# Kernel tuning notes

Hardware: AMD Instinct MI355X
Metric: run time of the kernel (lower is better)

## Reference

```python
import jax, jax.numpy as jnp
import numpy as np

# dims
B, V, IMG = 16, 2, 224
G, PATCH, SG = 7, 14, 16
D, NH, L = 768, 12, 12
DH = D // NH            # 64
P = DH // 4             # rope frequencies per axis (2D axial RoPE)
N = G * G               # 49 glimpse tokens
S = SG * SG             # 256 scene tokens
GSIZE = G * PATCH       # 98 px glimpse


def _ln(x, w, b):
    m = x.mean(-1, keepdims=True)
    v = ((x - m) ** 2).mean(-1, keepdims=True)
    return (x - m) * jax.lax.rsqrt(v + 1e-6) * w + b


def _rope(pos, periods):
    # pos [B,N,2] -> cos,sin [B,N,2P]  (x freqs then y freqs)
    ang = (pos[..., :, None] / periods).reshape(pos.shape[0], pos.shape[1], -1)
    return jnp.cos(ang), jnp.sin(ang)


def _apply_rope(x, cos, sin):
    # x [B,H,N,DH]; cos/sin [B,N,DH//2]
    c = cos[:, None, :, :]
    s = sin[:, None, :, :]
    xr = x.reshape(x.shape[0], x.shape[1], x.shape[2], DH // 2, 2)
    x1, x2 = xr[..., 0], xr[..., 1]
    return jnp.stack([x1 * c - x2 * s, x1 * s + x2 * c], -1).reshape(x.shape)


def _heads(x):
    return x.reshape(x.shape[0], x.shape[1], NH, DH).transpose(0, 2, 1, 3)


def _merge(x):
    return x.transpose(0, 2, 1, 3).reshape(x.shape[0], x.shape[2], D)


def _attn(q, k, v):
    a = jax.nn.softmax(jnp.einsum('bhqd,bhkd->bhqk', q, k) / jnp.sqrt(jnp.float32(DH)), axis=-1)
    return jnp.einsum('bhqk,bhkd->bhqd', a, v)


def _cross(xq, xkv, qw, qb, kvw, kvb, ow, ob, rq, rkv):
    q = _heads(xq @ qw.T + qb)
    kv = xkv @ kvw.T + kvb
    k, v = _heads(kv[..., :D]), _heads(kv[..., D:])
    q = _apply_rope(q, *rq)
    k = _apply_rope(k, *rkv)
    return _merge(_attn(q, k, v)) @ ow.T + ob


def _bilinear(img, py, px):
    # img [C,H,W], py/px [GSIZE] pixel coords -> [C,GSIZE,GSIZE]
    Hh, Ww = img.shape[1], img.shape[2]
    y0 = jnp.clip(jnp.floor(py), 0, Hh - 2).astype(jnp.int32)
    x0 = jnp.clip(jnp.floor(px), 0, Ww - 2).astype(jnp.int32)
    wy = jnp.clip(py - y0, 0.0, 1.0)[None, :, None]
    wx = jnp.clip(px - x0, 0.0, 1.0)[None, None, :]
    g0, g1 = img[:, y0, :], img[:, y0 + 1, :]
    v00, v01 = g0[:, :, x0], g0[:, :, x0 + 1]
    v10, v11 = g1[:, :, x0], g1[:, :, x0 + 1]
    return (v00 * (1 - wy) + v10 * wy) * (1 - wx) + (v01 * (1 - wy) + v11 * wy) * wx


def _extract(images, c, s):
    # crop a [-1,1]-normalized glimpse of half-width `scale` at `center`
    lin = jnp.linspace(-1.0, 1.0, GSIZE)
    gy = c[:, 1:2] + s[:, None] * lin
    gx = c[:, 0:1] + s[:, None] * lin
    py = (gy + 1.0) * 0.5 * (images.shape[2] - 1)
    px = (gx + 1.0) * 0.5 * (images.shape[3] - 1)
    return jax.vmap(_bilinear)(images, py, px)


def _forward(images, centers, scales, patch_w, patch_b, scene_tokens,
             ln1_w, ln1_b, ln2_w, ln2_b, qkv_w, qkv_b, attn_out_w, attn_out_b,
             mlp_w1, mlp_b1, mlp_w2, mlp_b2,
             read_q_w, read_q_b, read_kv_w, read_kv_b, read_out_w, read_out_b, read_gate,
             write_q_w, write_q_b, write_kv_w, write_kv_b, write_out_w, write_out_b, write_gate):
    periods = 100.0 ** (jnp.arange(P, dtype=jnp.float32) / P)
    lin_s = jnp.linspace(-1.0, 1.0, SG)
    ys, xs = jnp.meshgrid(lin_s, lin_s, indexing='ij')
    scene_pos = jnp.broadcast_to(jnp.stack([xs.ravel(), ys.ravel()], -1), (B, S, 2))
    scene_rope = _rope(scene_pos, periods)
    lin_g = jnp.linspace(-1.0, 1.0, G)
    yg, xg = jnp.meshgrid(lin_g, lin_g, indexing='ij')
    goffs = jnp.stack([xg.ravel(), yg.ravel()], -1)  # [N,2]

    scene = jnp.broadcast_to(scene_tokens, (B, S, D))
    for vp in range(V):
        glimpse = _extract(images, centers[vp], scales[vp])  # [B,3,98,98]
        t = jax.lax.conv_general_dilated(glimpse, patch_w, (PATCH, PATCH), 'VALID',
                                         dimension_numbers=('NCHW', 'OIHW', 'NCHW'))
        local = t.reshape(B, D, N).transpose(0, 2, 1) + patch_b  # [B,49,D]
        lpos = centers[vp][:, None, :] + scales[vp][:, None, None] * goffs
        lrope = _rope(lpos, periods)
        for i in range(L):
            local = local + read_gate[i] * _cross(local, scene,
                read_q_w[i], read_q_b[i], read_kv_w[i], read_kv_b[i],
                read_out_w[i], read_out_b[i], lrope, scene_rope)
            # ViT block with RoPE self-attention
            h = _ln(local, ln1_w[i], ln1_b[i])
            qkv = h @ qkv_w[i].T + qkv_b[i]
            q, k, v = _heads(qkv[..., :D]), _heads(qkv[..., D:2 * D]), _heads(qkv[..., 2 * D:])
            q = _apply_rope(q, *lrope)
            k = _apply_rope(k, *lrope)
            local = local + _merge(_attn(q, k, v)) @ attn_out_w[i].T + attn_out_b[i]
            h = _ln(local, ln2_w[i], ln2_b[i])
            local = local + jax.nn.gelu(h @ mlp_w1[i].T + mlp_b1[i]) @ mlp_w2[i].T + mlp_b2[i]
            scene = scene + write_gate[i] * _cross(scene, local,
                write_q_w[i], write_q_b[i], write_kv_w[i], write_kv_b[i],
                write_out_w[i], write_out_b[i], scene_rope, lrope)
    return scene  # [B,S,D]


def setup_inputs() -> dict:
    key = jax.random.key(0)
    ks = iter(jax.random.split(key, 40))
    std = 0.02
    d = {}
    d['images'] = jax.random.normal(next(ks), (B, 3, IMG, IMG), jnp.float32)
    d['centers'] = jax.random.uniform(next(ks), (V, B, 2), jnp.float32, -0.5, 0.5)
    d['scales'] = jax.random.uniform(next(ks), (V, B), jnp.float32, 0.2, 0.4)
    d['patch_w'] = jax.random.normal(next(ks), (D, 3, PATCH, PATCH), jnp.float32) * std
    d['patch_b'] = jnp.zeros((D,), jnp.float32)
    d['scene_tokens'] = jax.random.normal(next(ks), (1, S, D), jnp.float32) / jnp.sqrt(jnp.float32(D))
    d['ln1_w'] = jnp.ones((L, D), jnp.float32); d['ln1_b'] = jnp.zeros((L, D), jnp.float32)
    d['ln2_w'] = jnp.ones((L, D), jnp.float32); d['ln2_b'] = jnp.zeros((L, D), jnp.float32)
    d['qkv_w'] = jax.random.normal(next(ks), (L, 3 * D, D), jnp.float32) * std
    d['qkv_b'] = jnp.zeros((L, 3 * D), jnp.float32)
    d['attn_out_w'] = jax.random.normal(next(ks), (L, D, D), jnp.float32) * std
    d['attn_out_b'] = jnp.zeros((L, D), jnp.float32)
    d['mlp_w1'] = jax.random.normal(next(ks), (L, 4 * D, D), jnp.float32) * std
    d['mlp_b1'] = jnp.zeros((L, 4 * D), jnp.float32)
    d['mlp_w2'] = jax.random.normal(next(ks), (L, D, 4 * D), jnp.float32) * std
    d['mlp_b2'] = jnp.zeros((L, D), jnp.float32)
    for pre in ('read', 'write'):
        d[pre + '_q_w'] = jax.random.normal(next(ks), (L, D, D), jnp.float32) * std
        d[pre + '_q_b'] = jnp.zeros((L, D), jnp.float32)
        d[pre + '_kv_w'] = jax.random.normal(next(ks), (L, 2 * D, D), jnp.float32) * std
        d[pre + '_kv_b'] = jnp.zeros((L, 2 * D), jnp.float32)
        d[pre + '_out_w'] = jax.random.normal(next(ks), (L, D, D), jnp.float32) * std
        d[pre + '_out_b'] = jnp.zeros((L, D), jnp.float32)
        d[pre + '_gate'] = jax.random.normal(next(ks), (L, D), jnp.float32) * 0.1
    return d


def reference(images, centers, scales, patch_w, patch_b, scene_tokens,
              ln1_w, ln1_b, ln2_w, ln2_b, qkv_w, qkv_b, attn_out_w, attn_out_b,
              mlp_w1, mlp_b1, mlp_w2, mlp_b2,
              read_q_w, read_q_b, read_kv_w, read_kv_b, read_out_w, read_out_b, read_gate,
              write_q_w, write_q_b, write_kv_w, write_kv_b, write_out_w, write_out_b, write_gate):
    return _forward(images, centers, scales, patch_w, patch_b, scene_tokens,
                    ln1_w, ln1_b, ln2_w, ln2_b, qkv_w, qkv_b, attn_out_w, attn_out_b,
                    mlp_w1, mlp_b1, mlp_w2, mlp_b2,
                    read_q_w, read_q_b, read_kv_w, read_kv_b, read_out_w, read_out_b, read_gate,
                    write_q_w, write_q_b, write_kv_w, write_kv_b, write_out_w, write_out_b, write_gate)
```

## Files before the change

kernel.cpp:

```cpp
#include <hip/hip_runtime.h>

#define B_ 16
#define V_ 2
#define D_ 768
#define NH_ 12
#define L_ 12
#define DH_ 64
#define N_ 49
#define S_ 256

__device__ __forceinline__ unsigned short f2bf(float f) {
  unsigned int u = __builtin_bit_cast(unsigned int, f);
  u += 0x7fffu + ((u >> 16) & 1u);
  return (unsigned short)(u >> 16);
}
__device__ __forceinline__ float bf2f(unsigned short h) {
  unsigned int u = ((unsigned int)h) << 16;
  return __builtin_bit_cast(float, u);
}
__device__ __forceinline__ float bflo(unsigned int w) {
  return __builtin_bit_cast(float, w << 16);
}
__device__ __forceinline__ float bfhi(unsigned int w) {
  return __builtin_bit_cast(float, w & 0xffff0000u);
}
__device__ __forceinline__ unsigned int packbf2(float a, float b) {
  return (unsigned int)f2bf(a) | ((unsigned int)f2bf(b) << 16);
}

using bf16x8 = __attribute__((ext_vector_type(8))) __bf16;
using u16x8  = __attribute__((ext_vector_type(8))) unsigned short;
using f32x4  = __attribute__((ext_vector_type(4))) float;

__device__ __forceinline__ void g2l16(const unsigned short* g, unsigned short* l) {
  __builtin_amdgcn_global_load_lds(
      (const __attribute__((address_space(1))) unsigned int*)g,
      (__attribute__((address_space(3))) unsigned int*)l, 16, 0, 0);
}

template <int BM, int BN, int BK, bool SWZ>
__global__ __launch_bounds__(256) void gemm_v7(
    const unsigned short* __restrict__ A, int lda,
    const unsigned short* __restrict__ W, int ldw,
    const float* __restrict__ bias,
    float* __restrict__ Cf, unsigned short* __restrict__ Cb, int ldc,
    const float* __restrict__ res, const float* __restrict__ gate,
    float* __restrict__ stats,
    int M, int N, int K, int epi)
{
  __shared__ unsigned short As[2][BM * BK];
  __shared__ unsigned short Bs[2][BN * BK];
  constexpr int FM = BM / 32, FN = BN / 32;
  constexpr int CPR = BK / 8;
  constexpr int LPS = (BM + BN) * BK / 2048;
  int m0, n0;
  if (SWZ) {
    const int gx = gridDim.x;
    const int nwg = gx * gridDim.y;
    const int orig = blockIdx.y * gx + blockIdx.x;
    const int xcd = orig & 7, rem = orig >> 3;
    const int qq = nwg >> 3, rr = nwg & 7;
    const int wgid = (xcd < rr ? xcd * (qq + 1) : rr * (qq + 1) + (xcd - rr) * qq) + rem;
    m0 = (wgid % gx) * BM; n0 = (wgid / gx) * BN;
  } else {
    m0 = blockIdx.x * BM; n0 = blockIdx.y * BN;
  }
  const int tid = threadIdx.x, lane = tid & 63, wid = tid >> 6;
  const int wr = wid >> 1, wc = wid & 1;
  const int fr = lane & 15, kq8 = lane >> 4;

  f32x4 acc[FM][FN];
#pragma unroll
  for (int mi = 0; mi < FM; ++mi)
#pragma unroll
    for (int ni = 0; ni < FN; ++ni) acc[mi][ni] = f32x4{0.f, 0.f, 0.f, 0.f};

  auto stage = [&](int buf, int k0) {
    const unsigned short* Ab = A + (size_t)m0 * lda + k0;
    const unsigned short* Bb = W + (size_t)n0 * ldw + k0;
#pragma unroll
    for (int ra = 0; ra < BM * BK / 2048; ++ra) {
      int c = ra * 256 + tid;
      int row = c / CPR, slot = c % CPR;
      int gslot = slot ^ (row & 7);
      g2l16(Ab + (size_t)row * lda + gslot * 8, &As[buf][c * 8]);
    }
#pragma unroll
    for (int rb = 0; rb < BN * BK / 2048; ++rb) {
      int c = rb * 256 + tid;
      int row = c / CPR, slot = c % CPR;
      int gslot = slot ^ (row & 7);
      g2l16(Bb + (size_t)row * ldw + gslot * 8, &Bs[buf][c * 8]);
    }
  };

  const int nt = K / BK;
  stage(0, 0);
  int cur = 0;
  for (int t = 0; t < nt; ++t) {
    if (t + 1 < nt) {
      stage(cur ^ 1, (t + 1) * BK);
      asm volatile("s_waitcnt vmcnt(%0)" :: "i"(LPS) : "memory");
    } else {
      asm volatile("s_waitcnt vmcnt(0)" ::: "memory");
    }
    __builtin_amdgcn_s_barrier();
#pragma unroll
    for (int ks = 0; ks < BK / 32; ++ks) {
      bf16x8 av[FM], bv[FN];
#pragma unroll
      for (int mi = 0; mi < FM; ++mi) {
        int row = wr * (BM / 2) + mi * 16 + fr;
        int idx = row * BK + (((ks * 4 + kq8) ^ (row & 7)) << 3);
        av[mi] = __builtin_bit_cast(bf16x8, *(const u16x8*)&As[cur][idx]);
      }
#pragma unroll
      for (int ni = 0; ni < FN; ++ni) {
        int row = wc * (BN / 2) + ni * 16 + fr;
        int idx = row * BK + (((ks * 4 + kq8) ^ (row & 7)) << 3);
        bv[ni] = __builtin_bit_cast(bf16x8, *(const u16x8*)&Bs[cur][idx]);
      }
#pragma unroll
      for (int mi = 0; mi < FM; ++mi)
#pragma unroll
        for (int ni = 0; ni < FN; ++ni)
          acc[mi][ni] = __builtin_amdgcn_mfma_f32_16x16x32_bf16(av[mi], bv[ni], acc[mi][ni], 0, 0, 0);
    }
    __builtin_amdgcn_s_barrier();
    cur ^= 1;
  }

  const int er = (lane >> 4) * 4, ec = lane & 15;
#pragma unroll
  for (int mi = 0; mi < FM; ++mi) {
#pragma unroll
    for (int i = 0; i < 4; ++i) {
      int gr = m0 + wr * (BM / 2) + mi * 16 + er + i;
      float mu = 0.f, rs = 0.f;
      if (epi >= 3) {
        float su = stats[gr * 2], sq = stats[gr * 2 + 1];
        mu = su * (1.0f / 768.0f);
        rs = rsqrtf(fmaxf(sq * (1.0f / 768.0f) - mu * mu, 0.f) + 1e-6f);
      }
      float s = 0.f, q = 0.f;
#pragma unroll
      for (int ni = 0; ni < FN; ++ni) {
        int gc = n0 + wc * (BN / 2) + ni * 16 + ec;
        float bi = bias ? bias[gc] : 0.0f;
        float gg = gate ? gate[gc] : 1.0f;
        float v = acc[mi][ni][i];
        if (epi == 0) {
          v += bi;
        } else if (epi == 1) {
          v += bi;
          v = v / (1.0f + __expf(-1.59576912f * (v + 0.044715f * v * v * v)));
        } else if (epi == 2) {
          v += bi;
          if (gr < M) v = res[(size_t)gr * ldc + gc] + gg * v;
        } else {
          v = (v - mu * gg) * rs + bi;
          if (epi == 4)
            v = v / (1.0f + __expf(-1.59576912f * (v + 0.044715f * v * v * v)));
        }
        if (gr < M) {
          if (Cf) Cf[(size_t)gr * ldc + gc] = v;
          if (Cb) Cb[(size_t)gr * ldc + gc] = f2bf(v);
        }
        s += v; q += v * v;
      }
      if (epi == 2 && stats) {
#pragma unroll
        for (int off = 1; off <= 8; off <<= 1) {
          s += __shfl_xor(s, off);
          q += __shfl_xor(q, off);
        }
        if ((lane & 15) == 0 && gr < M) {
          atomicAdd(&stats[gr * 2], s);
          atomicAdd(&stats[gr * 2 + 1], q);
        }
      }
    }
  }
}

template <int LKPAD>
__global__ __launch_bounds__(256) void attn_mfma(
    const unsigned short* __restrict__ Q, int ldq, int qoff, int Lq,
    const unsigned short* __restrict__ KV, int ldkv, int koff, int voff, int Lk,
    const float* __restrict__ cq, const float* __restrict__ sq, int rbq,
    const float* __restrict__ ck, const float* __restrict__ sk, int rbk,
    unsigned short* __restrict__ Out)
{
  constexpr int NT = LKPAD / 16;
  constexpr int NKS = LKPAD / 32;
  __shared__ unsigned short Kb[LKPAD * 64];
  __shared__ unsigned short Vt[64 * LKPAD];
  __shared__ unsigned short Qs[4][16 * 64];
  __shared__ unsigned short Pl[4][16 * LKPAD];
  const int b = blockIdx.x / NH_, h = blockIdx.x - b * NH_;
  const int tid = threadIdx.x, lane = tid & 63, wid = tid >> 6;

  for (int idx = tid; idx < LKPAD * 32; idx += 256) {
    int t = idx >> 5, m = idx & 31;
    int d = 2 * m;
    int ksl = (t << 6) + (((m >> 2) ^ (t & 7)) << 3) + ((m & 3) << 1);
    int vs0 = d * LKPAD + (((t >> 3) ^ (d & 7)) << 3) + (t & 7);
    int vs1 = (d + 1) * LKPAD + (((t >> 3) ^ ((d + 1) & 7)) << 3) + (t & 7);
    if (t < Lk) {
      size_t rowb = ((size_t)b * Lk + t) * ldkv;
      unsigned int kw = *(const unsigned int*)(KV + rowb + koff + h * DH_ + d);
      unsigned int vw = *(const unsigned int*)(KV + rowb + voff + h * DH_ + d);
      float k1 = bflo(kw), k2 = bfhi(kw);
      size_t ri = (size_t)b * rbk + (size_t)t * 32 + m;
      float c = ck[ri], s = sk[ri];
      *(unsigned int*)&Kb[ksl] = packbf2((k1 * c - k2 * s) * 0.125f, (k1 * s + k2 * c) * 0.125f);
      Vt[vs0] = (unsigned short)(vw & 0xffff);
      Vt[vs1] = (unsigned short)(vw >> 16);
    } else {
      *(unsigned int*)&Kb[ksl] = 0;
      Vt[vs0] = 0; Vt[vs1] = 0;
    }
  }
  const int qbase = blockIdx.y * 64 + wid * 16;
  for (int idx = lane; idx < 16 * 32; idx += 64) {
    int r = idx >> 5, m = idx & 31;
    int gq = qbase + r;
    unsigned int qr = 0;
    if (gq < Lq) {
      unsigned int qw = *(const unsigned int*)(Q + ((size_t)b * Lq + gq) * ldq + qoff + h * DH_ + 2 * m);
      float q1 = bflo(qw), q2 = bfhi(qw);
      size_t ri = (size_t)b * rbq + (size_t)gq * 32 + m;
      float c = cq[ri], s = sq[ri];
      qr = packbf2(q1 * c - q2 * s, q1 * s + q2 * c);
    }
    *(unsigned int*)&Qs[wid][(r << 6) + (((m >> 2) ^ (r & 7)) << 3) + ((m & 3) << 1)] = qr;
  }
  __syncthreads();

  const int fr = lane & 15, g = lane >> 4;
  bf16x8 qa[2];
#pragma unroll
  for (int ks = 0; ks < 2; ++ks)
    qa[ks] = __builtin_bit_cast(bf16x8,
        *(const u16x8*)&Qs[wid][(fr << 6) + ((((ks << 2) + g) ^ (fr & 7)) << 3)]);

  f32x4 sv[NT];
  __builtin_amdgcn_s_setprio(1);
#pragma unroll
  for (int t = 0; t < NT; ++t) {
    int key = (t << 4) + fr;
    f32x4 a = {0.f, 0.f, 0.f, 0.f};
#pragma unroll
    for (int ks = 0; ks < 2; ++ks) {
      bf16x8 kb = __builtin_bit_cast(bf16x8,
          *(const u16x8*)&Kb[(key << 6) + ((((ks << 2) + g) ^ (key & 7)) << 3)]);
      a = __builtin_amdgcn_mfma_f32_16x16x32_bf16(qa[ks], kb, a, 0, 0, 0);
    }
    sv[t] = a;
  }
  __builtin_amdgcn_s_setprio(0);
#pragma unroll
  for (int t = 0; t < NT; ++t) {
    int key = (t << 4) + fr;
    if (key >= Lk) sv[t] = f32x4{-1e30f, -1e30f, -1e30f, -1e30f};
  }
  f32x4 mx = sv[0];
#pragma unroll
  for (int t = 1; t < NT; ++t)
#pragma unroll
    for (int i = 0; i < 4; ++i) mx[i] = fmaxf(mx[i], sv[t][i]);
#pragma unroll
  for (int off = 1; off <= 8; off <<= 1)
#pragma unroll
    for (int i = 0; i < 4; ++i) mx[i] = fmaxf(mx[i], __shfl_xor(mx[i], off));
  f32x4 sm = {0.f, 0.f, 0.f, 0.f};
#pragma unroll
  for (int t = 0; t < NT; ++t)
#pragma unroll
    for (int i = 0; i < 4; ++i) {
      float e = __expf(sv[t][i] - mx[i]);
      sv[t][i] = e;
      sm[i] += e;
    }
#pragma unroll
  for (int off = 1; off <= 8; off <<= 1)
#pragma unroll
    for (int i = 0; i < 4; ++i) sm[i] += __shfl_xor(sm[i], off);
  f32x4 inv;
#pragma unroll
  for (int i = 0; i < 4; ++i) inv[i] = 1.0f / sm[i];
#pragma unroll
  for (int t = 0; t < NT; ++t) {
    int key = (t << 4) + fr;
    int chunk = key >> 3;
#pragma unroll
    for (int i = 0; i < 4; ++i) {
      int row = (g << 2) + i;
      Pl[wid][row * LKPAD + ((chunk ^ (row & 7)) << 3) + (key & 7)] = f2bf(sv[t][i]);
    }
  }
  f32x4 oacc[4];
#pragma unroll
  for (int n = 0; n < 4; ++n) oacc[n] = f32x4{0.f, 0.f, 0.f, 0.f};
  __builtin_amdgcn_s_setprio(1);
#pragma unroll
  for (int ks = 0; ks < NKS; ++ks) {
    int chunk = (ks << 2) + g;
    bf16x8 pa = __builtin_bit_cast(bf16x8,
        *(const u16x8*)&Pl[wid][fr * LKPAD + ((chunk ^ (fr & 7)) << 3)]);
#pragma unroll
    for (int n = 0; n < 4; ++n) {
      int drow = (n << 4) + fr;
      bf16x8 vb = __builtin_bit_cast(bf16x8,
          *(const u16x8*)&Vt[drow * LKPAD + ((chunk ^ (drow & 7)) << 3)]);
      oacc[n] = __builtin_amdgcn_mfma_f32_16x16x32_bf16(pa, vb, oacc[n], 0, 0, 0);
    }
  }
  __builtin_amdgcn_s_setprio(0);
#pragma unroll
  for (int n = 0; n < 4; ++n)
#pragma unroll
    for (int i = 0; i < 4; ++i) {
      int gq = qbase + (g << 2) + i;
      if (gq < Lq)
        Out[((size_t)b * Lq + gq) * D_ + h * DH_ + (n << 4) + fr] = f2bf(oacc[n][i] * inv[i]);
    }
}

struct CvtA {
  const float* s[11];
  unsigned short* d[11];
  const float* g[11];
  unsigned int lsrc[11];
  unsigned int lstride[11];
  int blkEnd[11];
};
__global__ __launch_bounds__(256) void cvt_multi_k(CvtA c) {
  int bid = blockIdx.x;
  int seg = 0;
#pragma unroll
  for (int i = 0; i < 10; ++i) seg += (bid >= c.blkEnd[i]) ? 1 : 0;
  unsigned int e = (unsigned int)(bid - (seg ? c.blkEnd[seg - 1] : 0)) * 2048u
                   + (unsigned int)threadIdx.x * 8u;
  unsigned int l = e / c.lsrc[seg], r = e - l * c.lsrc[seg];
  const float* s = c.s[seg] + e;
  unsigned short* d = c.d[seg] + (size_t)l * c.lstride[seg] + r;
  f32x4 a = *(const f32x4*)s, b2 = *(const f32x4*)(s + 4);
  const float* gp = c.g[seg];
  if (gp) {
    unsigned int k = e % 768u;
    const float* gpp = gp + (size_t)l * 768u + k;
    f32x4 ga = *(const f32x4*)gpp, gb = *(const f32x4*)(gpp + 4);
    a.x *= ga.x; a.y *= ga.y; a.z *= ga.z; a.w *= ga.w;
    b2.x *= gb.x; b2.y *= gb.y; b2.z *= gb.z; b2.w *= gb.w;
  }
  u16x8 o;
  o[0] = f2bf(a.x); o[1] = f2bf(a.y); o[2] = f2bf(a.z); o[3] = f2bf(a.w);
  o[4] = f2bf(b2.x); o[5] = f2bf(b2.y); o[6] = f2bf(b2.z); o[7] = f2bf(b2.w);
  *(u16x8*)d = o;
}

__global__ __launch_bounds__(256) void foldprep_k(
    const float* __restrict__ qkvw, const float* __restrict__ qkvb,
    const float* __restrict__ g1, const float* __restrict__ b1,
    const float* __restrict__ m1w, const float* __restrict__ m1b,
    const float* __restrict__ g2, const float* __restrict__ b2,
    float* __restrict__ cq, float* __restrict__ bq,
    float* __restrict__ cm, float* __restrict__ bm)
{
  int row = blockIdx.x * 4 + (threadIdx.x >> 6);
  int lane = threadIdx.x & 63;
  const int QT = L_ * 2304;
  const float *wrow, *gv, *bv;
  float bb; float *co, *bo; int oi;
  if (row < QT) {
    int l = row / 2304, n = row - l * 2304;
    wrow = qkvw + ((size_t)l * 2304 + n) * 768;
    gv = g1 + l * 768; bv = b1 + l * 768;
    bb = qkvb[row]; co = cq; bo = bq; oi = row;
  } else {
    int r2 = row - QT;
    int l = r2 / 3072, n = r2 - l * 3072;
    wrow = m1w + ((size_t)l * 3072 + n) * 768;
    gv = g2 + l * 768; bv = b2 + l * 768;
    bb = m1b[r2]; co = cm; bo = bm; oi = r2;
  }
  float cs = 0.f, bs = 0.f;
#pragma unroll
  for (int j = 0; j < 12; ++j) {
    float w = wrow[lane + 64 * j];
    cs += w * gv[lane + 64 * j];
    bs += w * bv[lane + 64 * j];
  }
  for (int o = 32; o; o >>= 1) { cs += __shfl_xor(cs, o); bs += __shfl_xor(bs, o); }
  if (lane == 0) { co[oi] = cs; bo[oi] = bb + bs; }
}

__global__ void cvt_patch_k(const float* __restrict__ s, unsigned short* __restrict__ d) {
  int i = blockIdx.x * 256 + threadIdx.x;
  if (i >= 768 * 768) return;
  int r = i / 768, col = i - r * 768;
  d[i] = f2bf(col < 588 ? s[r * 588 + col] : 0.0f);
}

__global__ void fbias_k(const float* __restrict__ wqb, const float* __restrict__ rkvb,
                        float* __restrict__ fb) {
  int i = blockIdx.x * 256 + threadIdx.x;
  if (i >= L_ * 2304) return;
  int l = i / 2304, c = i - l * 2304;
  fb[i] = (c < 768) ? wqb[l * 768 + c] : rkvb[l * 1536 + (c - 768)];
}

__global__ void fbias2_k(const float* __restrict__ wkvb, const float* __restrict__ rqb,
                         float* __restrict__ fb2) {
  int i = blockIdx.x * 256 + threadIdx.x;
  if (i >= L_ * 2304) return;
  int l = i / 2304, c = i - l * 2304;
  fb2[i] = (c < 1536) ? wkvb[l * 1536 + c] : rqb[((l + 1) % L_) * 768 + (c - 1536)];
}

__global__ void init_scene_k(const float* __restrict__ tok, float* __restrict__ sf,
                             unsigned short* __restrict__ sb, int total) {
  int i = blockIdx.x * 256 + threadIdx.x;
  if (i < total) {
    float v = tok[i % (S_ * D_)];
    sf[i] = v; sb[i] = f2bf(v);
  }
}

__global__ void rope_scene_k(float* __restrict__ c, float* __restrict__ s) {
  int idx = blockIdx.x * 256 + threadIdx.x;
  if (idx >= S_ * 32) return;
  int t = idx >> 5, m = idx & 31;
  int i = t >> 4, j = t & 15;
  float xx = -1.0f + 2.0f * j / 15.0f;
  float yy = -1.0f + 2.0f * i / 15.0f;
  float coord = (m < 16) ? xx : yy;
  float per = powf(100.0f, (float)(m & 15) / 16.0f);
  float ang = coord / per;
  c[idx] = cosf(ang); s[idx] = sinf(ang);
}

__global__ void rope_local_k(float* __restrict__ c, float* __restrict__ s,
                             const float* __restrict__ ctr, const float* __restrict__ scl) {
  int idx = blockIdx.x * 256 + threadIdx.x;
  if (idx >= B_ * N_ * 32) return;
  int b = idx / (N_ * 32);
  int r = idx - b * (N_ * 32);
  int pch = r >> 5, m = r & 31;
  int py = pch / 7, px = pch - py * 7;
  float cx = ctr[b * 2], cy = ctr[b * 2 + 1], sc = scl[b];
  float gx = cx + sc * ((px - 3.0f) / 3.0f);
  float gy = cy + sc * ((py - 3.0f) / 3.0f);
  float coord = (m < 16) ? gx : gy;
  float per = powf(100.0f, (float)(m & 15) / 16.0f);
  float ang = coord / per;
  c[idx] = cosf(ang); s[idx] = sinf(ang);
}

__global__ void im2col_k(unsigned short* __restrict__ xb, const float* __restrict__ img,
                         const float* __restrict__ ctr, const float* __restrict__ scl) {
  int idx = blockIdx.x * 256 + threadIdx.x;
  if (idx >= 784 * 768) return;
  int row = idx / 768, col = idx - row * 768;
  float val = 0.0f;
  if (col < 588) {
    int b = row / 49, pch = row - b * 49;
    int c = col / 196, rr = col - c * 196;
    int i = rr / 14, j = rr - i * 14;
    int py = pch / 7, px = pch - py * 7;
    int gyi = py * 14 + i, gxi = px * 14 + j;
    float cx = ctr[b * 2], cy = ctr[b * 2 + 1], sc = scl[b];
    float gy = cy + sc * (-1.0f + 2.0f * gyi / 97.0f);
    float gx = cx + sc * (-1.0f + 2.0f * gxi / 97.0f);
    float pyi = (gy + 1.0f) * 0.5f * 223.0f;
    float pxi = (gx + 1.0f) * 0.5f * 223.0f;
    float y0f = fminf(fmaxf(floorf(pyi), 0.0f), 222.0f);
    float x0f = fminf(fmaxf(floorf(pxi), 0.0f), 222.0f);
    int y0 = (int)y0f, x0 = (int)x0f;
    float wy = fminf(fmaxf(pyi - y0f, 0.0f), 1.0f);
    float wx = fminf(fmaxf(pxi - x0f, 0.0f), 1.0f);
    const float* base = img + (size_t)(b * 3 + c) * 224 * 224;
    float v00 = base[y0 * 224 + x0],       v01 = base[y0 * 224 + x0 + 1];
    float v10 = base[(y0 + 1) * 224 + x0], v11 = base[(y0 + 1) * 224 + x0 + 1];
    val = (v00 * (1.0f - wy) + v10 * wy) * (1.0f - wx) + (v01 * (1.0f - wy) + v11 * wy) * wx;
  }
  xb[idx] = f2bf(val);
}

extern "C" void kernel_launch(void* const* d_in, const int* in_sizes, int n_in,
                              void* d_out, int out_size, void* d_ws, size_t ws_size,
                              hipStream_t stream) {
  const float* images    = (const float*)d_in[0];
  const float* centers   = (const float*)d_in[1];
  const float* scales    = (const float*)d_in[2];
  const float* patch_w   = (const float*)d_in[3];
  const float* patch_b   = (const float*)d_in[4];
  const float* scene_tok = (const float*)d_in[5];
  const float* ln1_w = (const float*)d_in[6];
  const float* ln1_b = (const float*)d_in[7];
  const float* ln2_w = (const float*)d_in[8];
  const float* ln2_b = (const float*)d_in[9];
  const float* qkv_w = (const float*)d_in[10];
  const float* qkv_b = (const float*)d_in[11];
  const float* ao_w  = (const float*)d_in[12];
  const float* ao_b  = (const float*)d_in[13];
  const float* m1_w  = (const float*)d_in[14];
  const float* m1_b  = (const float*)d_in[15];
  const float* m2_w  = (const float*)d_in[16];
  const float* m2_b  = (const float*)d_in[17];
  const float* rq_w  = (const float*)d_in[18];
  const float* rq_b  = (const float*)d_in[19];
  const float* rkv_w = (const float*)d_in[20];
  const float* rkv_b = (const float*)d_in[21];
  const float* ro_w  = (const float*)d_in[22];
  const float* ro_b  = (const float*)d_in[23];
  const float* rgate = (const float*)d_in[24];
  const float* wq_w  = (const float*)d_in[25];
  const float* wq_b  = (const float*)d_in[26];
  const float* wkv_w = (const float*)d_in[27];
  const float* wkv_b = (const float*)d_in[28];
  const float* wo_w  = (const float*)d_in[29];
  const float* wo_b  = (const float*)d_in[30];
  const float* wgate = (const float*)d_in[31];

  float* scene_f = (float*)d_out;

  char* p = (char*)d_ws;
  auto alloc = [&](size_t bytes) { char* r = p; p += (bytes + 255) & ~(size_t)255; return (void*)r; };
  unsigned short* scene_bf = (unsigned short*)alloc((size_t)4096 * 768 * 2);
  float*          local_f  = (float*)alloc((size_t)784 * 768 * 4);
  unsigned short* local_bf = (unsigned short*)alloc((size_t)896 * 768 * 2);
  unsigned short* q_r_bf   = (unsigned short*)alloc((size_t)896 * 768 * 2);
  unsigned short* qrkv_bf  = (unsigned short*)alloc((size_t)4096 * 2304 * 2);
  unsigned short* kv_bf    = (unsigned short*)alloc((size_t)896 * 2304 * 2);
  unsigned short* kvq_bf   = (unsigned short*)alloc((size_t)896 * 2304 * 2);
  unsigned short* act_bf   = (unsigned short*)alloc((size_t)4096 * 768 * 2);
  unsigned short* x_bf     = (unsigned short*)alloc((size_t)896 * 768 * 2);
  float* sc_cos = (float*)alloc((size_t)S_ * 32 * 4);
  float* sc_sin = (float*)alloc((size_t)S_ * 32 * 4);
  float* l_cos  = (float*)alloc((size_t)B_ * N_ * 32 * 4);
  float* l_sin  = (float*)alloc((size_t)B_ * N_ * 32 * 4);
  unsigned short* patch_wbf = (unsigned short*)alloc((size_t)768 * 768 * 2);
  float*          fb        = (float*)alloc((size_t)L_ * 2304 * 4);
  float*          fb2       = (float*)alloc((size_t)L_ * 2304 * 4);
  float*          cq_v      = (float*)alloc((size_t)L_ * 2304 * 4);
  float*          bq_v      = (float*)alloc((size_t)L_ * 2304 * 4);
  float*          cm_v      = (float*)alloc((size_t)L_ * 3072 * 4);
  float*          bm_v      = (float*)alloc((size_t)L_ * 3072 * 4);
  const size_t ST_SLICE = 896 * 2;
  float*          statsAll  = (float*)alloc((size_t)V_ * L_ * 2 * ST_SLICE * 4);

  static const size_t REGSZ[9] = {589824, 1769472, 589824, 1769472, 589824,
                                  2359296, 2359296, 1769472, 589824};
  struct SegDef { const float* src; int reg; unsigned off; unsigned lsrc; int nl; const float* gma; };
  const SegDef SEGS[11] = {
    {rq_w,            0, 0,       589824,  L_,    nullptr},
    {wq_w,            1, 0,       589824,  L_,    nullptr},
    {rkv_w,           1, 589824,  1179648, L_,    nullptr},
    {ro_w,            2, 0,       589824,  L_,    nullptr},
    {qkv_w,           3, 0,       1769472, L_,    ln1_w},
    {ao_w,            4, 0,       589824,  L_,    nullptr},
    {m1_w,            5, 0,       2359296, L_,    ln2_w},
    {m2_w,            6, 0,       2359296, L_,    nullptr},
    {wkv_w,           7, 0,       1179648, L_,    nullptr},
    {rq_w + 589824,   7, 1179648, 589824,  L_ - 1, nullptr},
    {wo_w,            8, 0,       589824,  L_,    nullptr},
  };
  size_t regBase[9];
  size_t perLayer = 0;
  {
    size_t cur = 0;
    for (int i = 0; i < 9; ++i) { regBase[i] = cur; cur += REGSZ[i] * L_; perLayer += REGSZ[i]; }
  }
  const size_t allElems = perLayer * L_;
  size_t usedBytes = (size_t)(p - (char*)d_ws);
  bool preconv = ws_size >= usedBytes + allElems * 2 + 4096;
  unsigned short* wbf = (unsigned short*)alloc((preconv ? allElems : perLayer) * 2);

  auto GQ = [&](const unsigned short* A, int lda, const unsigned short* Wp,
                const float* bias, float* Cf, unsigned short* Cb, int ldc,
                const float* res, const float* gt, int N, int epi) {
    gemm_v7<128, 128, 64, true><<<dim3(32, N / 128), 256, 0, stream>>>(
        A, lda, Wp, 768, bias, Cf, Cb, ldc, res, gt, nullptr, 4096, N, 768, epi);
  };
  auto GW = [&](const unsigned short* A, int lda, const unsigned short* Wp,
                const float* bias, float* Cf, unsigned short* Cb, int ldc,
                const float* res, const float* gt, int N, int epi) {
    gemm_v7<128, 64, 64, true><<<dim3(32, N / 64), 256, 0, stream>>>(
        A, lda, Wp, 768, bias, Cf, Cb, ldc, res, gt, nullptr, 4096, N, 768, epi);
  };
  auto GS = [&](const unsigned short* A, int lda, const unsigned short* Wp, int ldw,
                const float* bias, float* Cf, unsigned short* Cb, int ldc,
                const float* res, const float* gt, float* st, int N, int K, int epi) {
    gemm_v7<64, 64, 128, false><<<dim3(13, N / 64), 256, 0, stream>>>(
        A, lda, Wp, ldw, bias, Cf, Cb, ldc, res, gt, st, 784, N, K, epi);
  };

  {
    hipMemsetAsync(statsAll, 0, (size_t)V_ * L_ * 2 * ST_SLICE * 4, stream);
    int total = B_ * S_ * D_;
    init_scene_k<<<(total + 255) / 256, 256, 0, stream>>>(scene_tok, scene_f, scene_bf, total);
    rope_scene_k<<<(S_ * 32 + 255) / 256, 256, 0, stream>>>(sc_cos, sc_sin);
    cvt_patch_k<<<(768 * 768 + 255) / 256, 256, 0, stream>>>(patch_w, patch_wbf);
    fbias_k<<<(L_ * 2304 + 255) / 256, 256, 0, stream>>>(wq_b, rkv_b, fb);
    fbias2_k<<<(L_ * 2304 + 255) / 256, 256, 0, stream>>>(wkv_b, rq_b, fb2);
    foldprep_k<<<(L_ * (2304 + 3072)) / 4, 256, 0, stream>>>(
        qkv_w, qkv_b, ln1_w, ln1_b, m1_w, m1_b, ln2_w, ln2_b, cq_v, bq_v, cm_v, bm_v);
    if (preconv) {
      CvtA cv;
      int blk = 0;
      for (int i = 0; i < 11; ++i) {
        cv.s[i] = SEGS[i].src;
        cv.d[i] = wbf + regBase[SEGS[i].reg] + SEGS[i].off;
        cv.g[i] = SEGS[i].gma;
        cv.lsrc[i] = SEGS[i].lsrc;
        cv.lstride[i] = (unsigned)REGSZ[SEGS[i].reg];
        blk += (int)((size_t)SEGS[i].lsrc * SEGS[i].nl / 2048);
        cv.blkEnd[i] = blk;
      }
      cvt_multi_k<<<blk, 256, 0, stream>>>(cv);
    }
  }

  for (int vp = 0; vp < V_; ++vp) {
    const float* ctr = centers + (size_t)vp * B_ * 2;
    const float* scl = scales + (size_t)vp * B_;
    rope_local_k<<<(B_ * N_ * 32 + 255) / 256, 256, 0, stream>>>(l_cos, l_sin, ctr, scl);
    im2col_k<<<(784 * 768 + 255) / 256, 256, 0, stream>>>(x_bf, images, ctr, scl);
    GS(x_bf, 768, patch_wbf, 768, patch_b, local_f, local_bf, 768,
       nullptr, nullptr, nullptr, 768, 768, 0);

    for (int l = 0; l < L_; ++l) {
      const unsigned short* wR[9];
      if (preconv) {
        for (int rg = 0; rg < 9; ++rg)
          wR[rg] = wbf + regBase[rg] + (size_t)l * REGSZ[rg];
      } else {
        CvtA cv;
        int blk = 0;
        size_t cur = 0;
        size_t rb[9];
        for (int rg = 0; rg < 9; ++rg) { rb[rg] = cur; cur += REGSZ[rg]; wR[rg] = wbf + rb[rg]; }
        for (int i = 0; i < 11; ++i) {
          size_t srcl = (i == 9) ? (size_t)((l + 1) % L_) : (size_t)l;
          cv.s[i] = (i == 9 ? rq_w : SEGS[i].src) + srcl * SEGS[i].lsrc;
          cv.d[i] = wbf + rb[SEGS[i].reg] + SEGS[i].off;
          cv.g[i] = SEGS[i].gma ? SEGS[i].gma + srcl * 768 : nullptr;
          cv.lsrc[i] = SEGS[i].lsrc;
          cv.lstride[i] = (unsigned)REGSZ[SEGS[i].reg];
          blk += (int)(SEGS[i].lsrc / 2048);
          cv.blkEnd[i] = blk;
        }
        cvt_multi_k<<<blk, 256, 0, stream>>>(cv);
      }
      float* stats1 = statsAll + ((size_t)(vp * L_ + l) * 2 + 0) * ST_SLICE;
      float* stats2 = statsAll + ((size_t)(vp * L_ + l) * 2 + 1) * ST_SLICE;

      GQ(scene_bf, 768, wR[1], fb + (size_t)l * 2304,
         nullptr, qrkv_bf, 2304, nullptr, nullptr, 2304, 0);
      if (l == 0)
        GS(local_bf, 768, wR[0], 768, rq_b + l * 768,
           nullptr, q_r_bf, 768, nullptr, nullptr, nullptr, 768, 768, 0);
      if (l == 0)
        attn_mfma<256><<<dim3(B_ * NH_, 1), 256, 0, stream>>>(q_r_bf, 768, 0, 49,
            qrkv_bf, 2304, 768, 1536, 256, l_cos, l_sin, N_ * 32, sc_cos, sc_sin, 0, act_bf);
      else
        attn_mfma<256><<<dim3(B_ * NH_, 1), 256, 0, stream>>>(kvq_bf, 2304, 1536, 49,
            qrkv_bf, 2304, 768, 1536, 256, l_cos, l_sin, N_ * 32, sc_cos, sc_sin, 0, act_bf);
      GS(act_bf, 768, wR[2], 768, ro_b + l * 768,
         local_f, local_bf, 768, local_f, rgate + l * 768, stats1, 768, 768, 2);
      GS(local_bf, 768, wR[3], 768, bq_v + (size_t)l * 2304,
         nullptr, kv_bf, 2304, nullptr, cq_v + (size_t)l * 2304, stats1, 2304, 768, 3);
      attn_mfma<64><<<dim3(B_ * NH_, 1), 256, 0, stream>>>(kv_bf, 2304, 0, 49,
          kv_bf, 2304, 768, 1536, 49, l_cos, l_sin, N_ * 32, l_cos, l_sin, N_ * 32, act_bf);
      GS(act_bf, 768, wR[4], 768, ao_b + l * 768,
         local_f, local_bf, 768, local_f, nullptr, stats2, 768, 768, 2);
      GS(local_bf, 768, wR[5], 768, bm_v + (size_t)l * 3072,
         nullptr, act_bf, 3072, nullptr, cm_v + (size_t)l * 3072, stats2, 3072, 768, 4);
      GS(act_bf, 3072, wR[6], 3072, m2_b + l * 768,
         local_f, local_bf, 768, local_f, nullptr, nullptr, 768, 3072, 2);
      GS(local_bf, 768, wR[7], 768, fb2 + (size_t)l * 2304,
         nullptr, kvq_bf, 2304, nullptr, nullptr, nullptr, 2304, 768, 0);
      attn_mfma<64><<<dim3(B_ * NH_, 4), 256, 0, stream>>>(qrkv_bf, 2304, 0, 256,
          kvq_bf, 2304, 0, 768, 49, sc_cos, sc_sin, 0, l_cos, l_sin, N_ * 32, act_bf);
      GW(act_bf, 768, wR[8], wo_b + l * 768,
         scene_f, scene_bf, 768, scene_f, wgate + l * 768, 768, 2);
    }
  }
}
```

Measured before the change: 6.919 ms.

## Specialize GEMM epilogues at compile time and replace stats atomics with partial slots

Turns the GEMM epilogue selector into a template parameter so each launch compiles only its own branch. Per-row LayerNorm sum and sum-of-squares partials now go into per-column-block slots with plain stores, and the consumer sums them, replacing atomicAdd and the stats memset. The RoPE table for the local tokens is now computed inside the im2col kernel, removing one launch per view. XCD swizzle is enabled for the small GEMMs too, at the cost of more kernel instantiations and wider stats reads in the normalizing epilogues.

```diff
diff --git a/kernel.cpp b/kernel.cpp
--- a/kernel.cpp
+++ b/kernel.cpp
@@ -38,7 +38,7 @@
       (__attribute__((address_space(3))) unsigned int*)l, 16, 0, 0);
 }
 
-template <int BM, int BN, int BK, bool SWZ>
+template <int BM, int BN, int BK, int EPI>
 __global__ __launch_bounds__(256) void gemm_v7(
     const unsigned short* __restrict__ A, int lda,
     const unsigned short* __restrict__ W, int ldw,
@@ -46,7 +46,7 @@
     float* __restrict__ Cf, unsigned short* __restrict__ Cb, int ldc,
     const float* __restrict__ res, const float* __restrict__ gate,
     float* __restrict__ stats,
-    int M, int N, int K, int epi)
+    int M, int N, int K)
 {
   __shared__ unsigned short As[2][BM * BK];
   __shared__ unsigned short Bs[2][BN * BK];
@@ -54,7 +54,7 @@
   constexpr int CPR = BK / 8;
   constexpr int LPS = (BM + BN) * BK / 2048;
   int m0, n0;
-  if (SWZ) {
+  {
     const int gx = gridDim.x;
     const int nwg = gx * gridDim.y;
     const int orig = blockIdx.y * gx + blockIdx.x;
@@ -62,8 +62,6 @@
     const int qq = nwg >> 3, rr = nwg & 7;
     const int wgid = (xcd < rr ? xcd * (qq + 1) : rr * (qq + 1) + (xcd - rr) * qq) + rem;
     m0 = (wgid % gx) * BM; n0 = (wgid / gx) * BN;
-  } else {
-    m0 = blockIdx.x * BM; n0 = blockIdx.y * BN;
   }
   const int tid = threadIdx.x, lane = tid & 63, wid = tid >> 6;
   const int wr = wid >> 1, wc = wid & 1;
@@ -82,15 +80,13 @@
     for (int ra = 0; ra < BM * BK / 2048; ++ra) {
       int c = ra * 256 + tid;
       int row = c / CPR, slot = c % CPR;
-      int gslot = slot ^ (row & 7);
-      g2l16(Ab + (size_t)row * lda + gslot * 8, &As[buf][c * 8]);
+      g2l16(Ab + (size_t)row * lda + (slot ^ (row & 7)) * 8, &As[buf][c * 8]);
     }
 #pragma unroll
     for (int rb = 0; rb < BN * BK / 2048; ++rb) {
       int c = rb * 256 + tid;
       int row = c / CPR, slot = c % CPR;
-      int gslot = slot ^ (row & 7);
-      g2l16(Bb + (size_t)row * ldw + gslot * 8, &Bs[buf][c * 8]);
+      g2l16(Bb + (size_t)row * ldw + (slot ^ (row & 7)) * 8, &Bs[buf][c * 8]);
     }
   };
 
@@ -131,55 +127,84 @@
   }
 
   const int er = (lane >> 4) * 4, ec = lane & 15;
-#pragma unroll
-  for (int mi = 0; mi < FM; ++mi) {
-#pragma unroll
-    for (int i = 0; i < 4; ++i) {
-      int gr = m0 + wr * (BM / 2) + mi * 16 + er + i;
-      float mu = 0.f, rs = 0.f;
-      if (epi >= 3) {
-        float su = stats[gr * 2], sq = stats[gr * 2 + 1];
-        mu = su * (1.0f / 768.0f);
-        rs = rsqrtf(fmaxf(sq * (1.0f / 768.0f) - mu * mu, 0.f) + 1e-6f);
+  float mu_[FM][4], rs_[FM][4];
+  if constexpr (EPI >= 4) {
+#pragma unroll
+    for (int mi = 0; mi < FM; ++mi)
+#pragma unroll
+      for (int i = 0; i < 4; ++i) {
+        int gr = m0 + wr * (BM / 2) + mi * 16 + er + i;
+        float su = 0.f, sq = 0.f;
+        if (gr < M) {
+          const f32x4* sp = (const f32x4*)&stats[(size_t)gr * 48];
+#pragma unroll
+          for (int j = 0; j < 12; ++j) {
+            f32x4 v4 = sp[j];
+            su += v4.x + v4.z;
+            sq += v4.y + v4.w;
+          }
+        }
+        float mu = su * (1.0f / 768.0f);
+        mu_[mi][i] = mu;
+        rs_[mi][i] = rsqrtf(fmaxf(sq * (1.0f / 768.0f) - mu * mu, 0.f) + 1e-6f);
       }
-      float s = 0.f, q = 0.f;
-#pragma unroll
-      for (int ni = 0; ni < FN; ++ni) {
-        int gc = n0 + wc * (BN / 2) + ni * 16 + ec;
-        float bi = bias ? bias[gc] : 0.0f;
-        float gg = gate ? gate[gc] : 1.0f;
+  }
+  float ssum[FM][4], sqsum[FM][4];
+  if constexpr (EPI == 3) {
+#pragma unroll
+    for (int mi = 0; mi < FM; ++mi)
+#pragma unroll
+      for (int i = 0; i < 4; ++i) { ssum[mi][i] = 0.f; sqsum[mi][i] = 0.f; }
+  }
+#pragma unroll
+  for (int mi = 0; mi < FM; ++mi)
+#pragma unroll
+    for (int ni = 0; ni < FN; ++ni) {
+      int gc = n0 + wc * (BN / 2) + ni * 16 + ec;
+      float bi = bias ? bias[gc] : 0.0f;
+      float gg = gate ? gate[gc] : 1.0f;
+#pragma unroll
+      for (int i = 0; i < 4; ++i) {
+        int gr = m0 + wr * (BM / 2) + mi * 16 + er + i;
         float v = acc[mi][ni][i];
-        if (epi == 0) {
+        if constexpr (EPI == 0) {
           v += bi;
-        } else if (epi == 1) {
+        } else if constexpr (EPI == 1) {
           v += bi;
           v = v / (1.0f + __expf(-1.59576912f * (v + 0.044715f * v * v * v)));
-        } else if (epi == 2) {
+        } else if constexpr (EPI == 2 || EPI == 3) {
           v += bi;
           if (gr < M) v = res[(size_t)gr * ldc + gc] + gg * v;
         } else {
-          v = (v - mu * gg) * rs + bi;
-          if (epi == 4)
+          v = (v - mu_[mi][i] * gg) * rs_[mi][i] + bi;
+          if constexpr (EPI == 5)
             v = v / (1.0f + __expf(-1.59576912f * (v + 0.044715f * v * v * v)));
         }
         if (gr < M) {
           if (Cf) Cf[(size_t)gr * ldc + gc] = v;
           if (Cb) Cb[(size_t)gr * ldc + gc] = f2bf(v);
         }
-        s += v; q += v * v;
+        if constexpr (EPI == 3) { ssum[mi][i] += v; sqsum[mi][i] += v * v; }
       }
-      if (epi == 2 && stats) {
+    }
+  if constexpr (EPI == 3) {
+    const int nb = n0 >> 6;
+#pragma unroll
+    for (int mi = 0; mi < FM; ++mi)
+#pragma unroll
+      for (int i = 0; i < 4; ++i) {
+        float s = ssum[mi][i], q = sqsum[mi][i];
 #pragma unroll
         for (int off = 1; off <= 8; off <<= 1) {
           s += __shfl_xor(s, off);
           q += __shfl_xor(q, off);
         }
+        int gr = m0 + wr * (BM / 2) + mi * 16 + er + i;
         if ((lane & 15) == 0 && gr < M) {
-          atomicAdd(&stats[gr * 2], s);
-          atomicAdd(&stats[gr * 2 + 1], q);
+          stats[(size_t)gr * 48 + (nb * 2 + wc) * 2]     = s;
+          stats[(size_t)gr * 48 + (nb * 2 + wc) * 2 + 1] = q;
         }
       }
-    }
   }
 }
 
@@ -441,25 +466,9 @@
   c[idx] = cosf(ang); s[idx] = sinf(ang);
 }
 
-__global__ void rope_local_k(float* __restrict__ c, float* __restrict__ s,
-                             const float* __restrict__ ctr, const float* __restrict__ scl) {
-  int idx = blockIdx.x * 256 + threadIdx.x;
-  if (idx >= B_ * N_ * 32) return;
-  int b = idx / (N_ * 32);
-  int r = idx - b * (N_ * 32);
-  int pch = r >> 5, m = r & 31;
-  int py = pch / 7, px = pch - py * 7;
-  float cx = ctr[b * 2], cy = ctr[b * 2 + 1], sc = scl[b];
-  float gx = cx + sc * ((px - 3.0f) / 3.0f);
-  float gy = cy + sc * ((py - 3.0f) / 3.0f);
-  float coord = (m < 16) ? gx : gy;
-  float per = powf(100.0f, (float)(m & 15) / 16.0f);
-  float ang = coord / per;
-  c[idx] = cosf(ang); s[idx] = sinf(ang);
-}
-
 __global__ void im2col_k(unsigned short* __restrict__ xb, const float* __restrict__ img,
-                         const float* __restrict__ ctr, const float* __restrict__ scl) {
+                         const float* __restrict__ ctr, const float* __restrict__ scl,
+                         float* __restrict__ lc, float* __restrict__ ls) {
   int idx = blockIdx.x * 256 + threadIdx.x;
   if (idx >= 784 * 768) return;
   int row = idx / 768, col = idx - row * 768;
@@ -486,6 +495,19 @@
     val = (v00 * (1.0f - wy) + v10 * wy) * (1.0f - wx) + (v01 * (1.0f - wy) + v11 * wy) * wx;
   }
   xb[idx] = f2bf(val);
+  if (idx < B_ * N_ * 32) {
+    int b = idx / (N_ * 32);
+    int r = idx - b * (N_ * 32);
+    int pch = r >> 5, m = r & 31;
+    int py = pch / 7, px = pch - py * 7;
+    float cx = ctr[b * 2], cy = ctr[b * 2 + 1], sc = scl[b];
+    float gx = cx + sc * ((px - 3.0f) / 3.0f);
+    float gy = cy + sc * ((py - 3.0f) / 3.0f);
+    float coord = (m < 16) ? gx : gy;
+    float per = powf(100.0f, (float)(m & 15) / 16.0f);
+    float ang = coord / per;
+    lc[idx] = cosf(ang); ls[idx] = sinf(ang);
+  }
 }
 
 extern "C" void kernel_launch(void* const* d_in, const int* in_sizes, int n_in,
@@ -548,24 +570,24 @@
   float*          bq_v      = (float*)alloc((size_t)L_ * 2304 * 4);
   float*          cm_v      = (float*)alloc((size_t)L_ * 3072 * 4);
   float*          bm_v      = (float*)alloc((size_t)L_ * 3072 * 4);
-  const size_t ST_SLICE = 896 * 2;
-  float*          statsAll  = (float*)alloc((size_t)V_ * L_ * 2 * ST_SLICE * 4);
+  float*          stats1    = (float*)alloc((size_t)832 * 48 * 4);
+  float*          stats2    = (float*)alloc((size_t)832 * 48 * 4);
 
   static const size_t REGSZ[9] = {589824, 1769472, 589824, 1769472, 589824,
                                   2359296, 2359296, 1769472, 589824};
   struct SegDef { const float* src; int reg; unsigned off; unsigned lsrc; int nl; const float* gma; };
   const SegDef SEGS[11] = {
-    {rq_w,            0, 0,       589824,  L_,    nullptr},
-    {wq_w,            1, 0,       589824,  L_,    nullptr},
-    {rkv_w,           1, 589824,  1179648, L_,    nullptr},
-    {ro_w,            2, 0,       589824,  L_,    nullptr},
-    {qkv_w,           3, 0,       1769472, L_,    ln1_w},
-    {ao_w,            4, 0,       589824,  L_,    nullptr},
-    {m1_w,            5, 0,       2359296, L_,    ln2_w},
-    {m2_w,            6, 0,       2359296, L_,    nullptr},
-    {wkv_w,           7, 0,       1179648, L_,    nullptr},
+    {rq_w,            0, 0,       589824,  L_,     nullptr},
+    {wq_w,            1, 0,       589824,  L_,     nullptr},
+    {rkv_w,           1, 589824,  1179648, L_,     nullptr},
+    {ro_w,            2, 0,       589824,  L_,     nullptr},
+    {qkv_w,           3, 0,       1769472, L_,     ln1_w},
+    {ao_w,            4, 0,       589824,  L_,     nullptr},
+    {m1_w,            5, 0,       2359296, L_,     ln2_w},
+    {m2_w,            6, 0,       2359296, L_,     nullptr},
+    {wkv_w,           7, 0,       1179648, L_,     nullptr},
     {rq_w + 589824,   7, 1179648, 589824,  L_ - 1, nullptr},
-    {wo_w,            8, 0,       589824,  L_,    nullptr},
+    {wo_w,            8, 0,       589824,  L_,     nullptr},
   };
   size_t regBase[9];
   size_t perLayer = 0;
@@ -578,27 +600,7 @@
   bool preconv = ws_size >= usedBytes + allElems * 2 + 4096;
   unsigned short* wbf = (unsigned short*)alloc((preconv ? allElems : perLayer) * 2);
 
-  auto GQ = [&](const unsigned short* A, int lda, const unsigned short* Wp,
-                const float* bias, float* Cf, unsigned short* Cb, int ldc,
-                const float* res, const float* gt, int N, int epi) {
-    gemm_v7<128, 128, 64, true><<<dim3(32, N / 128), 256, 0, stream>>>(
-        A, lda, Wp, 768, bias, Cf, Cb, ldc, res, gt, nullptr, 4096, N, 768, epi);
-  };
-  auto GW = [&](const unsigned short* A, int lda, const unsigned short* Wp,
-                const float* bias, float* Cf, unsigned short* Cb, int ldc,
-                const float* res, const float* gt, int N, int epi) {
-    gemm_v7<128, 64, 64, true><<<dim3(32, N / 64), 256, 0, stream>>>(
-        A, lda, Wp, 768, bias, Cf, Cb, ldc, res, gt, nullptr, 4096, N, 768, epi);
-  };
-  auto GS = [&](const unsigned short* A, int lda, const unsigned short* Wp, int ldw,
-                const float* bias, float* Cf, unsigned short* Cb, int ldc,
-                const float* res, const float* gt, float* st, int N, int K, int epi) {
-    gemm_v7<64, 64, 128, false><<<dim3(13, N / 64), 256, 0, stream>>>(
-        A, lda, Wp, ldw, bias, Cf, Cb, ldc, res, gt, st, 784, N, K, epi);
-  };
-
   {
-    hipMemsetAsync(statsAll, 0, (size_t)V_ * L_ * 2 * ST_SLICE * 4, stream);
     int total = B_ * S_ * D_;
     init_scene_k<<<(total + 255) / 256, 256, 0, stream>>>(scene_tok, scene_f, scene_bf, total);
     rope_scene_k<<<(S_ * 32 + 255) / 256, 256, 0, stream>>>(sc_cos, sc_sin);
@@ -626,10 +628,10 @@
   for (int vp = 0; vp < V_; ++vp) {
     const float* ctr = centers + (size_t)vp * B_ * 2;
     const float* scl = scales + (size_t)vp * B_;
-    rope_local_k<<<(B_ * N_ * 32 + 255) / 256, 256, 0, stream>>>(l_cos, l_sin, ctr, scl);
-    im2col_k<<<(784 * 768 + 255) / 256, 256, 0, stream>>>(x_bf, images, ctr, scl);
-    GS(x_bf, 768, patch_wbf, 768, patch_b, local_f, local_bf, 768,
-       nullptr, nullptr, nullptr, 768, 768, 0);
+    im2col_k<<<(784 * 768 + 255) / 256, 256, 0, stream>>>(x_bf, images, ctr, scl, l_cos, l_sin);
+    gemm_v7<64, 64, 128, 0><<<dim3(13, 12), 256, 0, stream>>>(
+        x_bf, 768, patch_wbf, 768, patch_b, local_f, local_bf, 768,
+        nullptr, nullptr, nullptr, 784, 768, 768);
 
     for (int l = 0; l < L_; ++l) {
       const unsigned short* wR[9];
@@ -654,38 +656,45 @@
         }
         cvt_multi_k<<<blk, 256, 0, stream>>>(cv);
       }
-      float* stats1 = statsAll + ((size_t)(vp * L_ + l) * 2 + 0) * ST_SLICE;
-      float* stats2 = statsAll + ((size_t)(vp * L_ + l) * 2 + 1) * ST_SLICE;
-
-      GQ(scene_bf, 768, wR[1], fb + (size_t)l * 2304,
-         nullptr, qrkv_bf, 2304, nullptr, nullptr, 2304, 0);
+
+      gemm_v7<128, 128, 64, 0><<<dim3(32, 18), 256, 0, stream>>>(
+          scene_bf, 768, wR[1], 768, fb + (size_t)l * 2304,
+          nullptr, qrkv_bf, 2304, nullptr, nullptr, nullptr, 4096, 2304, 768);
       if (l == 0)
-        GS(local_bf, 768, wR[0], 768, rq_b + l * 768,
-           nullptr, q_r_bf, 768, nullptr, nullptr, nullptr, 768, 768, 0);
+        gemm_v7<64, 64, 128, 0><<<dim3(13, 12), 256, 0, stream>>>(
+            local_bf, 768, wR[0], 768, rq_b + l * 768,
+            nullptr, q_r_bf, 768, nullptr, nullptr, nullptr, 784, 768, 768);
       if (l == 0)
         attn_mfma<256><<<dim3(B_ * NH_, 1), 256, 0, stream>>>(q_r_bf, 768, 0, 49,
             qrkv_bf, 2304, 768, 1536, 256, l_cos, l_sin, N_ * 32, sc_cos, sc_sin, 0, act_bf);
       else
         attn_mfma<256><<<dim3(B_ * NH_, 1), 256, 0, stream>>>(kvq_bf, 2304, 1536, 49,
             qrkv_bf, 2304, 768, 1536, 256, l_cos, l_sin, N_ * 32, sc_cos, sc_sin, 0, act_bf);
-      GS(act_bf, 768, wR[2], 768, ro_b + l * 768,
-         local_f, local_bf, 768, local_f, rgate + l * 768, stats1, 768, 768, 2);
-      GS(local_bf, 768, wR[3], 768, bq_v + (size_t)l * 2304,
-         nullptr, kv_bf, 2304, nullptr, cq_v + (size_t)l * 2304, stats1, 2304, 768, 3);
+      gemm_v7<64, 64, 128, 3><<<dim3(13, 12), 256, 0, stream>>>(
+          act_bf, 768, wR[2], 768, ro_b + l * 768,
+          local_f, local_bf, 768, local_f, rgate + l * 768, stats1, 784, 768, 768);
+      gemm_v7<64, 64, 128, 4><<<dim3(13, 36), 256, 0, stream>>>(
+          local_bf, 768, wR[3], 768, bq_v + (size_t)l * 2304,
+          nullptr, kv_bf, 2304, nullptr, cq_v + (size_t)l * 2304, stats1, 784, 2304, 768);
       attn_mfma<64><<<dim3(B_ * NH_, 1), 256, 0, stream>>>(kv_bf, 2304, 0, 49,
           kv_bf, 2304, 768, 1536, 49, l_cos, l_sin, N_ * 32, l_cos, l_sin, N_ * 32, act_bf);
-      GS(act_bf, 768, wR[4], 768, ao_b + l * 768,
-         local_f, local_bf, 768, local_f, nullptr, stats2, 768, 768, 2);
-      GS(local_bf, 768, wR[5], 768, bm_v + (size_t)l * 3072,
-         nullptr, act_bf, 3072, nullptr, cm_v + (size_t)l * 3072, stats2, 3072, 768, 4);
-      GS(act_bf, 3072, wR[6], 3072, m2_b + l * 768,
-         local_f, local_bf, 768, local_f, nullptr, nullptr, 768, 3072, 2);
-      GS(local_bf, 768, wR[7], 768, fb2 + (size_t)l * 2304,
-         nullptr, kvq_bf, 2304, nullptr, nullptr, nullptr, 2304, 768, 0);
+      gemm_v7<64, 64, 128, 3><<<dim3(13, 12), 256, 0, stream>>>(
+          act_bf, 768, wR[4], 768, ao_b + l * 768,
+          local_f, local_bf, 768, local_f, nullptr, stats2, 784, 768, 768);
+      gemm_v7<64, 64, 128, 5><<<dim3(13, 48), 256, 0, stream>>>(
+          local_bf, 768, wR[5], 768, bm_v + (size_t)l * 3072,
+          nullptr, act_bf, 3072, nullptr, cm_v + (size_t)l * 3072, stats2, 784, 3072, 768);
+      gemm_v7<64, 64, 128, 2><<<dim3(13, 12), 256, 0, stream>>>(
+          act_bf, 3072, wR[6], 3072, m2_b + l * 768,
+          local_f, local_bf, 768, local_f, nullptr, nullptr, 784, 768, 3072);
+      gemm_v7<64, 64, 128, 0><<<dim3(13, 36), 256, 0, stream>>>(
+          local_bf, 768, wR[7], 768, fb2 + (size_t)l * 2304,
+          nullptr, kvq_bf, 2304, nullptr, nullptr, nullptr, 784, 2304, 768);
       attn_mfma<64><<<dim3(B_ * NH_, 4), 256, 0, stream>>>(qrkv_bf, 2304, 0, 256,
           kvq_bf, 2304, 0, 768, 49, sc_cos, sc_sin, 0, l_cos, l_sin, N_ * 32, act_bf);
-      GW(act_bf, 768, wR[8], wo_b + l * 768,
-         scene_f, scene_bf, 768, scene_f, wgate + l * 768, 768, 2);
-    }
-  }
-}
+      gemm_v7<128, 64, 64, 2><<<dim3(32, 12), 256, 0, stream>>>(
+          act_bf, 768, wR[8], 768, wo_b + l * 768,
+          scene_f, scene_bf, 768, scene_f, wgate + l * 768, nullptr, 4096, 768, 768);
+    }
+  }
+}
```

Measured after the change: 6.119 ms. 11.6% less time.
